# Performance work log

Measured on AMD Instinct MI355X. Metric: run time of the kernel, lower is better.

## Reference

```python
import jax, jax.numpy as jnp
import numpy as np

B, C, H, W = 4, 8, 384, 384
CHANS = 18  # MLP hidden width (module default chans=18)
BAND = 32   # half-width of acquired low-frequency band


def setup_inputs() -> dict:
    key = jax.random.key(0)
    ks = jax.random.split(key, 8)
    acquired_kspace = jax.random.normal(ks[0], (B, C, H, W, 2), jnp.float32)
    acquiring_kspace = jax.random.normal(ks[1], (B, C, H, W, 2), jnp.float32)
    mid = W // 2
    am = np.zeros((B, W), np.float32)
    am[:, mid - BAND:mid + BAND] = 1.0  # acquired center band -> left/right well-defined
    acquired_mask = jnp.asarray(am)
    qm = np.zeros((B, W), np.float32)
    qm[:, ::24] = 1.0  # columns currently being acquired
    acquiring_mask = jnp.asarray(qm)
    CH = C * H
    IN = 2 * CH  # concat(acquiring_features, acquired_features)
    # MLP: Linear(IN,CHANS)+ReLU, Linear(CHANS,CHANS)+ReLU x2, Linear(CHANS,1)+Sigmoid (pools=4 layers)
    W1 = jax.random.normal(ks[2], (CHANS, IN), jnp.float32) * 0.02
    b1 = jnp.zeros((CHANS,), jnp.float32)
    W2 = jax.random.normal(ks[3], (CHANS, CHANS), jnp.float32) * 0.02
    b2 = jnp.zeros((CHANS,), jnp.float32)
    W3 = jax.random.normal(ks[4], (CHANS, CHANS), jnp.float32) * 0.02
    b3 = jnp.zeros((CHANS,), jnp.float32)
    W4 = jax.random.normal(ks[5], (1, CHANS), jnp.float32) * 0.02
    b4 = jnp.zeros((1,), jnp.float32)
    return dict(acquired_kspace=acquired_kspace, acquiring_kspace=acquiring_kspace,
                acquired_mask=acquired_mask, acquiring_mask=acquiring_mask,
                W1=W1, b1=b1, W2=W2, b2=b2, W3=W3, b3=b3, W4=W4, b4=b4)


def reference(acquired_kspace, acquiring_kspace, acquired_mask, acquiring_mask,
              W1, b1, W2, b2, W3, b3, W4, b4):
    cabs = lambda x: jnp.sqrt(jnp.sum(x * x, axis=-1))  # complex magnitude of trailing (re,im)
    # per-column flattened features, row-major over (C,H) like torch.flatten: [B, W, C*H]
    Fq = cabs(acquiring_kspace).transpose(0, 3, 1, 2).reshape(B, W, -1)
    Fa = cabs(acquired_kspace).transpose(0, 3, 1, 2).reshape(B, W, -1)
    CH = Fq.shape[-1]
    # split first linear over the concat([acquiring, acquired]) input
    Pq = Fq @ W1[:, :CH].T   # [B, W_i, CHANS]
    Pa = Fa @ W1[:, CH:].T   # [B, W_c, CHANS]
    h = jax.nn.relu(Pq[:, :, None, :] + Pa[:, None, :, :] + b1)  # [B, W_i, W_c, CHANS]
    h = jax.nn.relu(h @ W2.T + b2)
    h = jax.nn.relu(h @ W3.T + b3)
    out = jax.nn.sigmoid(h @ W4.T + b4)[..., 0]  # [B, W_i, W_c]
    # faithful left/right bounds from acquired_mask (same as torch.nonzero(...)[0][0])
    mid = W // 2
    right = mid + jnp.argmax(acquired_mask[:, mid:] < 1.0, axis=1)              # [B]
    left = jnp.argmax(acquired_mask[:, :mid][:, ::-1] < 1.0, axis=1) + 1        # [B]
    c = jnp.arange(W)
    cmask = (c[None, :] >= left[:, None]) & (c[None, :] < right[:, None])       # [B, W_c]
    denom = (right - left).astype(out.dtype)
    heat = jnp.sum(out * cmask[:, None, :].astype(out.dtype), axis=2) / denom[:, None]
    heat = jnp.where(acquiring_mask > 0, heat, jnp.zeros_like(heat))            # only nonzero acquiring cols
    return jnp.broadcast_to(heat[:, None, :], (B, H, W))  # torch.cat of h copies along dim=1
```

## Files before the change

### kernel.cpp

```cpp
#include <hip/hip_runtime.h>
#include <math.h>
#include <limits.h>

#define kB 4
#define kC 8
#define kH 384
#define kW 384
#define kCH (kC * kH)
#define kIN (2 * kCH)
#define kNC 18
#define kMID (kW / 2)

#define NCH 32
#define RPC (kCH / NCH)
#define NGRP 48
#define kN (kB * kW * kNC)

#define E18(M) M(0) M(1) M(2) M(3) M(4) M(5) M(6) M(7) M(8) M(9) M(10) M(11) M(12) M(13) M(14) M(15) M(16) M(17)
#define E3(M) M(0) M(1) M(2)

__device__ __forceinline__ void mask_bounds(const float* __restrict__ amb,
                                            int lane, int* left, int* right) {
    unsigned long long mR0 = __ballot(amb[kMID + lane] < 1.0f);
    unsigned long long mR1 = __ballot(amb[kMID + 64 + lane] < 1.0f);
    unsigned long long mR2 = __ballot(amb[kMID + 128 + lane] < 1.0f);
    unsigned long long mL0 = __ballot(amb[kMID - 1 - lane] < 1.0f);
    unsigned long long mL1 = __ballot(amb[kMID - 65 - lane] < 1.0f);
    unsigned long long mL2 = __ballot(amb[kMID - 129 - lane] < 1.0f);
    int candR = mR0 ? __builtin_ctzll(mR0)
              : (mR1 ? 64 + __builtin_ctzll(mR1)
              : (mR2 ? 128 + __builtin_ctzll(mR2) : 0));
    int candL = mL0 ? __builtin_ctzll(mL0)
              : (mL1 ? 64 + __builtin_ctzll(mL1)
              : (mL2 ? 128 + __builtin_ctzll(mL2) : 0));
    *left  = candL + 1;
    *right = kMID + candR;
}

__device__ __forceinline__ int nth_set(const unsigned long long* m, int n) {
#pragma unroll
    for (int j = 0; j < 6; ++j) {
        int p = __popcll(m[j]);
        if (n < p) {
            unsigned long long x = m[j];
            for (int t = 0; t < n; ++t) x &= (x - 1);
            return 64 * j + (int)__builtin_ctzll(x);
        }
        n -= p;
    }
    return -1;
}

__global__ __launch_bounds__(256)
void proj_kernel(const float* __restrict__ acquired,
                 const float* __restrict__ acquiring,
                 const float* __restrict__ am,
                 const float* __restrict__ qm,
                 const float* __restrict__ W1,
                 float* __restrict__ Pq_part, float* __restrict__ Pa_part,
                 float* __restrict__ out) {
    int g = blockIdx.x;
    int chunk = blockIdx.y & (NCH - 1);
    int pass = blockIdx.y >> 5;
    int b = blockIdx.z;
    int tid = threadIdx.x;
    int r0 = chunk * RPC;

    {
        int flatB = (blockIdx.z * gridDim.y + blockIdx.y) * gridDim.x + blockIdx.x;
        int gid = flatB * 256 + tid;
        if (gid < kB * kH * kW) {
            int w = gid % kW;
            int ob = gid / (kH * kW);
            if (!(qm[ob * kW + w] > 0.0f)) out[gid] = 0.0f;
        }
    }

    int lane = tid & 63;
    int c8 = tid & 7, r32 = tid >> 3;
    int wave = tid >> 6;

    __shared__ float sW[RPC][20];
    __shared__ float sRed[4][8][kNC];
    __shared__ int sCol[8];

    int wcol;
    bool slot_ok;
    if (pass == 0) {
        int left, right;
        mask_bounds(am + b * kW, lane, &left, &right);
        int w0 = g * 8;
        if (!((left < w0 + 8) && (right > w0))) return;
        wcol = w0 + c8;
        slot_ok = true;
    } else {
        unsigned long long qmm[6];
#pragma unroll
        for (int j = 0; j < 6; ++j)
            qmm[j] = __ballot(qm[b * kW + 64 * j + lane] > 0.0f);
        int totp = 0;
#pragma unroll
        for (int j = 0; j < 6; ++j) totp += __popcll(qmm[j]);
        if (8 * g >= totp) return;
        int found = nth_set(qmm, 8 * g + c8);
        slot_ok = (found >= 0);
        wcol = slot_ok ? found : 0;
    }
    if (tid < 8) sCol[tid] = slot_ok ? wcol : -1;

    const float* ks = (pass == 0) ? acquired : acquiring;
    const float* w1 = (pass == 0) ? (W1 + kCH) : W1;

    const float* colp = ks + ((size_t)(b * kCH + r0 + r32) * kW + wcol) * 2;
#define KLOAD(it) const float2 v##it = *reinterpret_cast<const float2*>(colp + (size_t)(it) * 32 * kW * 2);
    E3(KLOAD)

    for (int t = tid; t < kNC * RPC; t += 256) {
        int j = t / RPC, i = t - j * RPC;
        sW[i][j] = w1[j * kIN + r0 + i];
    }
    __syncthreads();

#define KMAG(it) const float f##it = sqrtf(v##it.x * v##it.x + v##it.y * v##it.y);
    E3(KMAG)

#define PDECL(j) float a##j = 0.0f;
    E18(PDECL)

#define ROWF(it) { \
        const float* row = &sW[r32 + 32 * (it)][0]; \
        const float4 q0 = *reinterpret_cast<const float4*>(row); \
        const float4 q1 = *reinterpret_cast<const float4*>(row + 4); \
        const float4 q2 = *reinterpret_cast<const float4*>(row + 8); \
        const float4 q3 = *reinterpret_cast<const float4*>(row + 12); \
        const float2 q4 = *reinterpret_cast<const float2*>(row + 16); \
        const float f = f##it; \
        a0  = fmaf(f, q0.x, a0);  a1  = fmaf(f, q0.y, a1);  \
        a2  = fmaf(f, q0.z, a2);  a3  = fmaf(f, q0.w, a3);  \
        a4  = fmaf(f, q1.x, a4);  a5  = fmaf(f, q1.y, a5);  \
        a6  = fmaf(f, q1.z, a6);  a7  = fmaf(f, q1.w, a7);  \
        a8  = fmaf(f, q2.x, a8);  a9  = fmaf(f, q2.y, a9);  \
        a10 = fmaf(f, q2.z, a10); a11 = fmaf(f, q2.w, a11); \
        a12 = fmaf(f, q3.x, a12); a13 = fmaf(f, q3.y, a13); \
        a14 = fmaf(f, q3.z, a14); a15 = fmaf(f, q3.w, a15); \
        a16 = fmaf(f, q4.x, a16); a17 = fmaf(f, q4.y, a17); }
    E3(ROWF)

#define WRED(j) { a##j += __shfl_down(a##j, 32, 64); a##j += __shfl_down(a##j, 16, 64); \
                  a##j += __shfl_down(a##j, 8, 64); }
    E18(WRED)
    if (lane < 8) {
#define SSTORE(j) sRed[wave][lane][j] = a##j;
        E18(SSTORE)
    }
    __syncthreads();
    if (tid < 8 * kNC) {
        int c = tid / kNC, j = tid - c * kNC;
        int wc = sCol[c];
        if (wc >= 0) {
            float s = sRed[0][c][j] + sRed[1][c][j] + sRed[2][c][j] + sRed[3][c][j];
            float* Pp = (pass == 0) ? Pa_part : Pq_part;
            Pp[((size_t)chunk * kB * kW + (size_t)b * kW + wc) * kNC + j] = s;
        }
    }
}

__global__ __launch_bounds__(256)
void reduce_kernel(const float* __restrict__ Pa_part, const float* __restrict__ Pq_part,
                   float* __restrict__ Pa, float* __restrict__ Pq) {
    int idx = blockIdx.x * 256 + threadIdx.x;
    if (idx >= 2 * kN) return;
    const float* src = (idx < kN) ? Pa_part : Pq_part;
    float* dst = (idx < kN) ? Pa : Pq;
    int n = (idx < kN) ? idx : idx - kN;
    float s = 0.0f;
#pragma unroll
    for (int c = 0; c < NCH; ++c) s += src[(size_t)c * kN + n];
    dst[n] = s;
}

__global__ __launch_bounds__(256)
void pair_kernel(const float* __restrict__ Pq, const float* __restrict__ Pa,
                 const float* __restrict__ am, const float* __restrict__ qmask,
                 const float* __restrict__ b1, const float* __restrict__ W2,
                 const float* __restrict__ b2, const float* __restrict__ W3,
                 const float* __restrict__ b3, const float* __restrict__ W4,
                 const float* __restrict__ b4, float* __restrict__ out) {
    int wi = blockIdx.x, b = blockIdx.y, tid = threadIdx.x;
    if (!(qmask[b * kW + wi] > 0.0f)) return;

    int lane = tid & 63, wave = tid >> 6;
    int left, right;
    mask_bounds(am + b * kW, lane, &left, &right);
    int span = right - left;

    __shared__ float sPa[kW][19];
    __shared__ float2 sW2[kNC * kNC / 2], sW3[kNC * kNC / 2];
    __shared__ float sW4[kNC], sb1[kNC], sb2[kNC], sb3[kNC], sPq[kNC];
    __shared__ float sb4s, wred[4], sHeat;

    if (tid < kNC * kNC / 2) {
        sW2[tid] = reinterpret_cast<const float2*>(W2)[tid];
        sW3[tid] = reinterpret_cast<const float2*>(W3)[tid];
    }
    if (tid >= 192 && tid < 192 + kNC) {
        int j = tid - 192;
        sPq[j] = Pq[((size_t)(b * kW + wi)) * kNC + j];
        sW4[j] = W4[j]; sb1[j] = b1[j]; sb2[j] = b2[j]; sb3[j] = b3[j];
    }
    if (tid == 255) sb4s = b4[0];

    for (int t = tid; t < span * kNC; t += 256) {
        int k = t / kNC, j = t - k * kNC;
        sPa[k][j] = Pa[((size_t)(b * kW + left + k)) * kNC + j];
    }
    __syncthreads();

#define DOT2(S, k, v) (S[(k)*9+0].x*v##0  + S[(k)*9+0].y*v##1  + \
                       S[(k)*9+1].x*v##2  + S[(k)*9+1].y*v##3  + \
                       S[(k)*9+2].x*v##4  + S[(k)*9+2].y*v##5  + \
                       S[(k)*9+3].x*v##6  + S[(k)*9+3].y*v##7  + \
                       S[(k)*9+4].x*v##8  + S[(k)*9+4].y*v##9  + \
                       S[(k)*9+5].x*v##10 + S[(k)*9+5].y*v##11 + \
                       S[(k)*9+6].x*v##12 + S[(k)*9+6].y*v##13 + \
                       S[(k)*9+7].x*v##14 + S[(k)*9+7].y*v##15 + \
                       S[(k)*9+8].x*v##16 + S[(k)*9+8].y*v##17)

    float ssum = 0.0f;
    for (int k = tid; k < span; k += 256) {
        const float* pa = &sPa[k][0];
#define L1(j) float x##j = fmaxf(sPq[j] + sb1[j] + pa[j], 0.0f);
        E18(L1)
        asm volatile("" ::: "memory");
#define L2(k) float y##k = fmaxf(sb2[k] + DOT2(sW2, k, x), 0.0f);
        E18(L2)
        asm volatile("" ::: "memory");
#define L3(k) float z##k = fmaxf(sb3[k] + DOT2(sW3, k, y), 0.0f);
        E18(L3)
        asm volatile("" ::: "memory");
        float t = sb4s +
            (sW4[0]*z0 + sW4[1]*z1 + sW4[2]*z2 + sW4[3]*z3 + sW4[4]*z4 + sW4[5]*z5 +
             sW4[6]*z6 + sW4[7]*z7 + sW4[8]*z8 + sW4[9]*z9 + sW4[10]*z10 + sW4[11]*z11 +
             sW4[12]*z12 + sW4[13]*z13 + sW4[14]*z14 + sW4[15]*z15 + sW4[16]*z16 + sW4[17]*z17);
        ssum += 1.0f / (1.0f + expf(-t));
    }

    ssum += __shfl_down(ssum, 32, 64); ssum += __shfl_down(ssum, 16, 64);
    ssum += __shfl_down(ssum,  8, 64); ssum += __shfl_down(ssum,  4, 64);
    ssum += __shfl_down(ssum,  2, 64); ssum += __shfl_down(ssum,  1, 64);
    if (lane == 0) wred[wave] = ssum;
    __syncthreads();
    if (tid == 0)
        sHeat = (wred[0] + wred[1] + wred[2] + wred[3]) / (float)span;
    __syncthreads();

    float hv = sHeat;
    for (int h = tid; h < kH; h += 256)
        out[((size_t)b * kH + h) * kW + wi] = hv;
}

extern "C" void kernel_launch(void* const* d_in, const int* in_sizes, int n_in,
                              void* d_out, int out_size, void* d_ws, size_t ws_size,
                              hipStream_t stream) {
    const float* acquired       = (const float*)d_in[0];
    const float* acquiring      = (const float*)d_in[1];
    const float* acquired_mask  = (const float*)d_in[2];
    const float* acquiring_mask = (const float*)d_in[3];
    const float* W1 = (const float*)d_in[4];
    const float* b1 = (const float*)d_in[5];
    const float* W2 = (const float*)d_in[6];
    const float* b2 = (const float*)d_in[7];
    const float* W3 = (const float*)d_in[8];
    const float* b3 = (const float*)d_in[9];
    const float* W4 = (const float*)d_in[10];
    const float* b4 = (const float*)d_in[11];
    float* out = (float*)d_out;

    float* Pa_part = (float*)d_ws;
    float* Pq_part = Pa_part + (size_t)NCH * kN;
    float* Pa      = Pq_part + (size_t)NCH * kN;
    float* Pq      = Pa + kN;

    proj_kernel<<<dim3(NGRP, 2 * NCH, kB), 256, 0, stream>>>(
        acquired, acquiring, acquired_mask, acquiring_mask, W1, Pq_part, Pa_part, out);
    reduce_kernel<<<(2 * kN + 255) / 256, 256, 0, stream>>>(Pa_part, Pq_part, Pa, Pq);
    pair_kernel<<<dim3(kW, kB), 256, 0, stream>>>(
        Pq, Pa, acquired_mask, acquiring_mask,
        b1, W2, b2, W3, b3, W4, b4, out);
}
```

Baseline: 152.9 us.

## Widen column groups from 8 to 32 columns per block in projection kernel

Each block now handles 32 columns with 8 rows per pass instead of 8 columns with 32 rows, so each thread loads and accumulates 12 rows rather than 3. Wider column groups make the global loads more contiguous (32 adjacent float2 per row) and reuse each shared-memory weight row across more columns, and the cross-lane reduction drops to a single shuffle. The trade-offs are fewer blocks (grid x shrinks from 48 to 12), coarser skipping of acquired-band groups (more wasted columns outside the band), a partially filled block for the 16 acquiring columns, and more registers per thread.

```diff
diff --git a/kernel.cpp b/kernel.cpp
--- a/kernel.cpp
+++ b/kernel.cpp
@@ -13,11 +13,12 @@
 
 #define NCH 32
 #define RPC (kCH / NCH)
-#define NGRP 48
+#define CPG 32
+#define NGRP (kW / CPG)
 #define kN (kB * kW * kNC)
 
 #define E18(M) M(0) M(1) M(2) M(3) M(4) M(5) M(6) M(7) M(8) M(9) M(10) M(11) M(12) M(13) M(14) M(15) M(16) M(17)
-#define E3(M) M(0) M(1) M(2)
+#define E12(M) M(0) M(1) M(2) M(3) M(4) M(5) M(6) M(7) M(8) M(9) M(10) M(11)
 
 __device__ __forceinline__ void mask_bounds(const float* __restrict__ amb,
                                             int lane, int* left, int* right) {
@@ -77,21 +78,21 @@
     }
 
     int lane = tid & 63;
-    int c8 = tid & 7, r32 = tid >> 3;
+    int c32 = tid & 31, r8 = tid >> 5;
     int wave = tid >> 6;
 
     __shared__ float sW[RPC][20];
-    __shared__ float sRed[4][8][kNC];
-    __shared__ int sCol[8];
+    __shared__ float sRed[4][CPG][kNC];
+    __shared__ int sCol[CPG];
 
     int wcol;
     bool slot_ok;
     if (pass == 0) {
         int left, right;
         mask_bounds(am + b * kW, lane, &left, &right);
-        int w0 = g * 8;
-        if (!((left < w0 + 8) && (right > w0))) return;
-        wcol = w0 + c8;
+        int w0 = g * CPG;
+        if (!((left < w0 + CPG) && (right > w0))) return;
+        wcol = w0 + c32;
         slot_ok = true;
     } else {
         unsigned long long qmm[6];
@@ -101,19 +102,19 @@
         int totp = 0;
 #pragma unroll
         for (int j = 0; j < 6; ++j) totp += __popcll(qmm[j]);
-        if (8 * g >= totp) return;
-        int found = nth_set(qmm, 8 * g + c8);
+        if (CPG * g >= totp) return;
+        int found = nth_set(qmm, CPG * g + c32);
         slot_ok = (found >= 0);
         wcol = slot_ok ? found : 0;
     }
-    if (tid < 8) sCol[tid] = slot_ok ? wcol : -1;
+    if (tid < CPG) sCol[tid] = slot_ok ? wcol : -1;
 
     const float* ks = (pass == 0) ? acquired : acquiring;
     const float* w1 = (pass == 0) ? (W1 + kCH) : W1;
 
-    const float* colp = ks + ((size_t)(b * kCH + r0 + r32) * kW + wcol) * 2;
-#define KLOAD(it) const float2 v##it = *reinterpret_cast<const float2*>(colp + (size_t)(it) * 32 * kW * 2);
-    E3(KLOAD)
+    const float* colp = ks + ((size_t)(b * kCH + r0 + r8) * kW + wcol) * 2;
+#define KLOAD(it) const float2 v##it = *reinterpret_cast<const float2*>(colp + (size_t)(it) * 8 * kW * 2);
+    E12(KLOAD)
 
     for (int t = tid; t < kNC * RPC; t += 256) {
         int j = t / RPC, i = t - j * RPC;
@@ -122,13 +123,13 @@
     __syncthreads();
 
 #define KMAG(it) const float f##it = sqrtf(v##it.x * v##it.x + v##it.y * v##it.y);
-    E3(KMAG)
+    E12(KMAG)
 
 #define PDECL(j) float a##j = 0.0f;
     E18(PDECL)
 
 #define ROWF(it) { \
-        const float* row = &sW[r32 + 32 * (it)][0]; \
+        const float* row = &sW[r8 + 8 * (it)][0]; \
         const float4 q0 = *reinterpret_cast<const float4*>(row); \
         const float4 q1 = *reinterpret_cast<const float4*>(row + 4); \
         const float4 q2 = *reinterpret_cast<const float4*>(row + 8); \
@@ -144,18 +145,17 @@
         a12 = fmaf(f, q3.x, a12); a13 = fmaf(f, q3.y, a13); \
         a14 = fmaf(f, q3.z, a14); a15 = fmaf(f, q3.w, a15); \
         a16 = fmaf(f, q4.x, a16); a17 = fmaf(f, q4.y, a17); }
-    E3(ROWF)
-
-#define WRED(j) { a##j += __shfl_down(a##j, 32, 64); a##j += __shfl_down(a##j, 16, 64); \
-                  a##j += __shfl_down(a##j, 8, 64); }
+    E12(ROWF)
+
+#define WRED(j) { a##j += __shfl_down(a##j, 32, 64); }
     E18(WRED)
-    if (lane < 8) {
+    if (lane < CPG) {
 #define SSTORE(j) sRed[wave][lane][j] = a##j;
         E18(SSTORE)
     }
     __syncthreads();
-    if (tid < 8 * kNC) {
-        int c = tid / kNC, j = tid - c * kNC;
+    for (int t = tid; t < CPG * kNC; t += 256) {
+        int c = t / kNC, j = t - c * kNC;
         int wc = sCol[c];
         if (wc >= 0) {
             float s = sRed[0][c][j] + sRed[1][c][j] + sRed[2][c][j] + sRed[3][c][j];
```

New measurement: 145.1 us. 1.05x faster.
